# Performance work log

Measured on AMD Instinct MI355X. Metric: run time of the kernel, lower is better.

## Reference

```python
import jax, jax.numpy as jnp
import numpy as np
import math

N = 50000          # n_nodes
E = 1600000        # n_edges (avg degree 32)
D = 256            # input_size
H = 8              # n_heads
HS = D // H        # head_size = 32


def setup_inputs() -> dict:
    key = jax.random.key(0)
    k1, k2, k3, k4, k5 = jax.random.split(key, 5)
    X = jax.random.normal(k1, (N, D), dtype=jnp.float32)
    # xavier_uniform for [D, HS] weight: bound = sqrt(6 / (fan_in + fan_out))
    bound = math.sqrt(6.0 / (D + HS))
    Wq = jax.random.uniform(k2, (D, HS), jnp.float32, -bound, bound)
    Wk = jax.random.uniform(k3, (D, HS), jnp.float32, -bound, bound)
    Wv = jax.random.uniform(k4, (D, HS), jnp.float32, -bound, bound)
    edge_index = jax.random.randint(k5, (2, E), 0, N, dtype=jnp.int32)
    return {"X": X, "Wq": Wq, "Wk": Wk, "Wv": Wv, "edge_index": edge_index}


def reference(X, Wq, Wk, Wv, edge_index):
    # Projections: [N, HS]
    Q = X @ Wq
    K = X @ Wk
    V = X @ Wv
    r = edge_index[0]  # row (query) node per edge
    c = edge_index[1]  # col (key/value) node per edge
    dk = jnp.asarray(math.sqrt(HS), dtype=X.dtype)
    # Edge-level attention logits: [E]
    scores = jnp.sum(Q[r] * K[c], axis=-1) / dk
    # Sparse row-wise (dim=1) softmax over existing edges only.
    row_max = jax.ops.segment_max(scores, r, num_segments=N)   # -inf for empty rows
    ex = jnp.exp(scores - row_max[r])                          # [E]
    denom = jax.ops.segment_sum(ex, r, num_segments=N)         # [N]
    # Weighted V aggregation: [N, HS]
    num = jax.ops.segment_sum(ex[:, None] * V[c], r, num_segments=N)
    # Rows with no incident edges produce zeros (matches sparse softmax + to_dense @ V).
    safe = jnp.maximum(denom, jnp.asarray(1e-30, X.dtype))[:, None]
    return jnp.where(denom[:, None] > 0, num / safe, jnp.zeros_like(num))
```

## Files before the change

### kernel.cpp

```cpp
#include <hip/hip_runtime.h>

#define N_NODES 50000
#define N_EDGES 1600000
#define D_IN    256
#define HS      32

#define NB      400
#define ROWS_PB 125
#define CAP     5120
#define EPB     4096

#define MTILE   64
#define XPITCH  264

typedef __bf16 bf16x8 __attribute__((ext_vector_type(8)));
typedef float  floatx4 __attribute__((ext_vector_type(4)));

static __device__ __forceinline__ unsigned short f2bf(float f) {
    unsigned u = __float_as_uint(f);
    return (unsigned short)((u + 0x7FFFu + ((u >> 16) & 1u)) >> 16);
}

__global__ __launch_bounds__(256) void wfrag_kernel(
    const float* __restrict__ Wq, const float* __restrict__ Wk,
    const float* __restrict__ Wv, unsigned short* __restrict__ wfrag)
{
    const int i = blockIdx.x * blockDim.x + threadIdx.x;
    if (i >= 8 * 6 * 64 * 8) return;
    const int j    = i & 7;
    const int lane = (i >> 3) & 63;
    const int st   = i >> 9;
    const int t    = st % 6;
    const int s    = st / 6;
    const int k    = s * 32 + (lane >> 4) * 8 + j;
    const int col  = t * 16 + (lane & 15);
    float v;
    if      (col < 32) v = Wq[k * HS + col];
    else if (col < 64) v = Wk[k * HS + (col - 32)];
    else               v = Wv[k * HS + (col - 64)];
    wfrag[i] = f2bf(v);
}

__global__ __launch_bounds__(256) void proj_mfma_kernel(
    const float* __restrict__ X, const unsigned short* __restrict__ wfrag,
    float* __restrict__ Q, unsigned int* __restrict__ KVp)
{
    __shared__ unsigned short xs[MTILE * XPITCH];

    const int t    = threadIdx.x;
    const int lane = t & 63;
    const int w    = t >> 6;
    const int quad = lane >> 4;
    const int m16  = lane & 15;
    const int row0 = blockIdx.x * MTILE;

#pragma unroll
    for (int it = 0; it < (MTILE * 64) / 256; it++) {
        const int idx = it * 256 + t;
        const int r   = idx >> 6;
        const int c4  = idx & 63;
        int gr = row0 + r;
        if (gr >= N_NODES) gr = N_NODES - 1;
        const float4 xv = *(const float4*)(X + (size_t)gr * D_IN + c4 * 4);
        ushort4 b;
        b.x = f2bf(xv.x); b.y = f2bf(xv.y); b.z = f2bf(xv.z); b.w = f2bf(xv.w);
        *(ushort4*)(&xs[r * XPITCH + c4 * 4]) = b;
    }
    __syncthreads();

    floatx4 acc[6];
#pragma unroll
    for (int nt = 0; nt < 6; nt++) acc[nt] = (floatx4)0.f;

    const int arow = w * 16 + m16;

#pragma unroll
    for (int s = 0; s < 8; s++) {
        bf16x8 bfr[6];
#pragma unroll
        for (int nt = 0; nt < 6; nt++)
            bfr[nt] = *(const bf16x8*)(wfrag + (((s * 6 + nt) * 64 + lane) * 8));
        const bf16x8 afr = *(const bf16x8*)(&xs[arow * XPITCH + s * 32 + quad * 8]);
#pragma unroll
        for (int nt = 0; nt < 6; nt++)
            acc[nt] = __builtin_amdgcn_mfma_f32_16x16x32_bf16(afr, bfr[nt], acc[nt], 0, 0, 0);
    }

#pragma unroll
    for (int i = 0; i < 4; i++) {
        const int gr = row0 + w * 16 + quad * 4 + i;
        if (gr < N_NODES) {
#pragma unroll
            for (int nt = 0; nt < 2; nt++)
                Q[gr * HS + nt * 16 + m16] = acc[nt][i];
#pragma unroll
            for (int p = 0; p < 2; p++) {
                const int j = p * 16 + m16;
                const unsigned kb = f2bf(acc[2 + p][i]);
                const unsigned vb = f2bf(acc[4 + p][i]);
                KVp[gr * HS + j] = (kb << 16) | vb;
            }
        }
    }
}

__global__ __launch_bounds__(256) void bin_kernel(
    const int* __restrict__ er, const int* __restrict__ ec,
    int* __restrict__ fill, unsigned int* __restrict__ pairs)
{
    __shared__ int lcnt[NB];
    const int t  = threadIdx.x;
    const int e0 = blockIdx.x * EPB;
    const int e1 = min(e0 + EPB, N_EDGES);

    for (int b = t; b < NB; b += 256) lcnt[b] = 0;
    __syncthreads();

    for (int e = e0 + t; e < e1; e += 256)
        atomicAdd(&lcnt[er[e] / ROWS_PB], 1);
    __syncthreads();

    for (int b = t; b < NB; b += 256) {
        const int c = lcnt[b];
        lcnt[b] = (c > 0) ? atomicAdd(&fill[b], c) : 0;
    }
    __syncthreads();

    for (int e = e0 + t; e < e1; e += 256) {
        const int r = er[e];
        const int b = r / ROWS_PB;
        const int slot = atomicAdd(&lcnt[b], 1);
        pairs[(size_t)b * CAP + slot] =
            ((unsigned)(r - b * ROWS_PB) << 16) | (unsigned)ec[e];
    }
}

__global__ __launch_bounds__(512) void scanfill_kernel(
    const int* __restrict__ fill, int* __restrict__ bstart,
    int* __restrict__ rowptr)
{
    __shared__ int s[512];
    const int t = threadIdx.x;
    const int v = (t < NB) ? fill[t] : 0;
    s[t] = v;
    __syncthreads();
#pragma unroll
    for (int ofs = 1; ofs < 512; ofs <<= 1) {
        const int u = (t >= ofs) ? s[t - ofs] : 0;
        __syncthreads();
        s[t] += u;
        __syncthreads();
    }
    if (t < NB) bstart[t] = s[t] - v;
    if (t == 0) rowptr[N_NODES] = N_EDGES;
}

__global__ __launch_bounds__(256) void place_kernel(
    const unsigned int* __restrict__ pairs, const int* __restrict__ fill,
    const int* __restrict__ bstart, int* __restrict__ rowptr,
    int* __restrict__ col_sorted)
{
    __shared__ int cnt_l[ROWS_PB];
    __shared__ int s[128];
    __shared__ int stage[CAP];

    const int b = blockIdx.x;
    const int t = threadIdx.x;
    const int n = fill[b];
    const int base = bstart[b];
    const unsigned int* pb = pairs + (size_t)b * CAP;

    for (int i = t; i < ROWS_PB; i += 256) cnt_l[i] = 0;
    __syncthreads();

    for (int i = t; i < n; i += 256)
        atomicAdd(&cnt_l[pb[i] >> 16], 1);
    __syncthreads();

    if (t < 128) s[t] = (t < ROWS_PB) ? cnt_l[t] : 0;
    __syncthreads();
#pragma unroll
    for (int ofs = 1; ofs < 128; ofs <<= 1) {
        const int u = (t < 128 && t >= ofs) ? s[t - ofs] : 0;
        __syncthreads();
        if (t < 128) s[t] += u;
        __syncthreads();
    }
    int excl = 0;
    if (t < ROWS_PB) {
        excl = s[t] - cnt_l[t];
        rowptr[b * ROWS_PB + t] = base + excl;
    }
    __syncthreads();
    if (t < ROWS_PB) cnt_l[t] = excl;
    __syncthreads();

    for (int i = t; i < n; i += 256) {
        const unsigned p = pb[i];
        const int pos = atomicAdd(&cnt_l[p >> 16], 1);
        stage[pos] = (int)(p & 0xFFFFu);
    }
    __syncthreads();

    for (int i = t; i < n; i += 256)
        col_sorted[base + i] = stage[i];
}

__global__ __launch_bounds__(256) void aggregate_kernel(
    const int* __restrict__ rowptr, const int* __restrict__ col,
    const float* __restrict__ Q, const unsigned int* __restrict__ KVp,
    float* __restrict__ out)
{
    const int lane = threadIdx.x & 63;
    const int r    = (blockIdx.x * blockDim.x + threadIdx.x) >> 6;
    if (r >= N_NODES) return;
    const int comp = lane & 7;
    const int slot = lane >> 3;

    const float4 q4 = *(const float4*)(Q + r * HS + comp * 4);
    const int start = rowptr[r];
    const int end   = rowptr[r + 1];
    const float scale = 0.17677669529663687f;

    float accD = 0.f;
    float n0 = 0.f, n1 = 0.f, n2 = 0.f, n3 = 0.f;

    for (int e0 = start; e0 < end; e0 += 16) {
        const int last = end - 1;
        const int eA = e0 + slot;
        const int eB = e0 + 8 + slot;
        const int cA = col[min(eA, last)];
        const int cB = col[min(eB, last)];
        const uint4 kvA = *(const uint4*)(KVp + (size_t)cA * HS + comp * 4);
        const uint4 kvB = *(const uint4*)(KVp + (size_t)cB * HS + comp * 4);

        float pA = q4.x * __uint_as_float(kvA.x & 0xFFFF0000u)
                 + q4.y * __uint_as_float(kvA.y & 0xFFFF0000u)
                 + q4.z * __uint_as_float(kvA.z & 0xFFFF0000u)
                 + q4.w * __uint_as_float(kvA.w & 0xFFFF0000u);
        float pB = q4.x * __uint_as_float(kvB.x & 0xFFFF0000u)
                 + q4.y * __uint_as_float(kvB.y & 0xFFFF0000u)
                 + q4.z * __uint_as_float(kvB.z & 0xFFFF0000u)
                 + q4.w * __uint_as_float(kvB.w & 0xFFFF0000u);
#pragma unroll
        for (int ofs = 1; ofs < 8; ofs <<= 1) {
            pA += __shfl_xor(pA, ofs, 64);
            pB += __shfl_xor(pB, ofs, 64);
        }
        const float exA = (eA < end) ? __expf(pA * scale) : 0.f;
        const float exB = (eB < end) ? __expf(pB * scale) : 0.f;
        accD += exA + exB;
        n0 += exA * __uint_as_float(kvA.x << 16) + exB * __uint_as_float(kvB.x << 16);
        n1 += exA * __uint_as_float(kvA.y << 16) + exB * __uint_as_float(kvB.y << 16);
        n2 += exA * __uint_as_float(kvA.z << 16) + exB * __uint_as_float(kvB.z << 16);
        n3 += exA * __uint_as_float(kvA.w << 16) + exB * __uint_as_float(kvB.w << 16);
    }

#pragma unroll
    for (int ofs = 8; ofs < 64; ofs <<= 1) {
        accD += __shfl_xor(accD, ofs, 64);
        n0 += __shfl_xor(n0, ofs, 64);
        n1 += __shfl_xor(n1, ofs, 64);
        n2 += __shfl_xor(n2, ofs, 64);
        n3 += __shfl_xor(n3, ofs, 64);
    }

    if (slot == 0) {
        const float inv = (accD > 0.f) ? 1.f / accD : 0.f;
        float4 o;
        o.x = n0 * inv; o.y = n1 * inv; o.z = n2 * inv; o.w = n3 * inv;
        *(float4*)(out + r * HS + comp * 4) = o;
    }
}

extern "C" void kernel_launch(void* const* d_in, const int* in_sizes, int n_in,
                              void* d_out, int out_size, void* d_ws, size_t ws_size,
                              hipStream_t stream)
{
    const float* X  = (const float*)d_in[0];
    const float* Wq = (const float*)d_in[1];
    const float* Wk = (const float*)d_in[2];
    const float* Wv = (const float*)d_in[3];
    const int*   ei = (const int*)d_in[4];
    const int* er = ei;
    const int* ec = ei + N_EDGES;

    float* out = (float*)d_out;

    float* Q          = (float*)d_ws;
    unsigned int* KVp = (unsigned int*)(Q + (size_t)N_NODES * HS);
    int* fill         = (int*)(KVp + (size_t)N_NODES * HS);
    int* bstart       = fill + NB;
    int* rowptr       = bstart + NB;
    unsigned short* wfrag = (unsigned short*)(rowptr + (N_NODES + 1));
    unsigned int* pairs   = (unsigned int*)(wfrag + 8 * 6 * 64 * 8);
    int* col_sorted   = (int*)(pairs + (size_t)NB * CAP);

    hipMemsetAsync(fill, 0, NB * sizeof(int), stream);

    wfrag_kernel<<<(8 * 6 * 64 * 8 + 255) / 256, 256, 0, stream>>>(Wq, Wk, Wv, wfrag);
    proj_mfma_kernel<<<(N_NODES + MTILE - 1) / MTILE, 256, 0, stream>>>(X, wfrag, Q, KVp);

    bin_kernel<<<(N_EDGES + EPB - 1) / EPB, 256, 0, stream>>>(er, ec, fill, pairs);
    scanfill_kernel<<<1, 512, 0, stream>>>(fill, bstart, rowptr);
    place_kernel<<<NB, 256, 0, stream>>>(pairs, fill, bstart, rowptr, col_sorted);

    aggregate_kernel<<<(N_NODES * 64 + 255) / 256, 256, 0, stream>>>(
        rowptr, col_sorted, Q, KVp, out);
}
```

Measured before the change: 177.3 us.

## Fold memset into wfrag kernel, cache edges in registers, deepen aggregate loads

Drops the separate memset and does the fill-counter zeroing and the rowptr sentinel write inside wfrag_kernel. bin_kernel and place_kernel keep each thread's edges in register arrays so the second pass does not reload them from global memory. aggregate_kernel now processes 32 edges per iteration and issues four independent gathers before computing, which gives more memory-level parallelism. The fixed register arrays (16 and 20 entries) assume EPB and CAP bounds and raise register pressure.

```diff
diff --git a/kernel.cpp b/kernel.cpp
--- a/kernel.cpp
+++ b/kernel.cpp
@@ -23,8 +23,13 @@
 
 __global__ __launch_bounds__(256) void wfrag_kernel(
     const float* __restrict__ Wq, const float* __restrict__ Wk,
-    const float* __restrict__ Wv, unsigned short* __restrict__ wfrag)
-{
+    const float* __restrict__ Wv, unsigned short* __restrict__ wfrag,
+    int* __restrict__ fill, int* __restrict__ rowptr)
+{
+    if (blockIdx.x == 0) {
+        for (int b = threadIdx.x; b < NB; b += 256) fill[b] = 0;
+        if (threadIdx.x == 0) rowptr[N_NODES] = N_EDGES;
+    }
     const int i = blockIdx.x * blockDim.x + threadIdx.x;
     if (i >= 8 * 6 * 64 * 8) return;
     const int j    = i & 7;
@@ -116,8 +121,16 @@
     for (int b = t; b < NB; b += 256) lcnt[b] = 0;
     __syncthreads();
 
-    for (int e = e0 + t; e < e1; e += 256)
-        atomicAdd(&lcnt[er[e] / ROWS_PB], 1);
+    int rl[16], cl[16];
+#pragma unroll
+    for (int i = 0; i < 16; i++) {
+        const int e = e0 + t + i * 256;
+        if (e < e1) {
+            rl[i] = er[e];
+            cl[i] = ec[e];
+            atomicAdd(&lcnt[rl[i] / ROWS_PB], 1);
+        }
+    }
     __syncthreads();
 
     for (int b = t; b < NB; b += 256) {
@@ -126,18 +139,21 @@
     }
     __syncthreads();
 
-    for (int e = e0 + t; e < e1; e += 256) {
-        const int r = er[e];
-        const int b = r / ROWS_PB;
-        const int slot = atomicAdd(&lcnt[b], 1);
-        pairs[(size_t)b * CAP + slot] =
-            ((unsigned)(r - b * ROWS_PB) << 16) | (unsigned)ec[e];
+#pragma unroll
+    for (int i = 0; i < 16; i++) {
+        const int e = e0 + t + i * 256;
+        if (e < e1) {
+            const int r = rl[i];
+            const int b = r / ROWS_PB;
+            const int slot = atomicAdd(&lcnt[b], 1);
+            pairs[(size_t)b * CAP + slot] =
+                ((unsigned)(r - b * ROWS_PB) << 16) | (unsigned)cl[i];
+        }
     }
 }
 
 __global__ __launch_bounds__(512) void scanfill_kernel(
-    const int* __restrict__ fill, int* __restrict__ bstart,
-    int* __restrict__ rowptr)
+    const int* __restrict__ fill, int* __restrict__ bstart)
 {
     __shared__ int s[512];
     const int t = threadIdx.x;
@@ -152,7 +168,6 @@
         __syncthreads();
     }
     if (t < NB) bstart[t] = s[t] - v;
-    if (t == 0) rowptr[N_NODES] = N_EDGES;
 }
 
 __global__ __launch_bounds__(256) void place_kernel(
@@ -173,8 +188,15 @@
     for (int i = t; i < ROWS_PB; i += 256) cnt_l[i] = 0;
     __syncthreads();
 
-    for (int i = t; i < n; i += 256)
-        atomicAdd(&cnt_l[pb[i] >> 16], 1);
+    unsigned pl[20];
+#pragma unroll
+    for (int k = 0; k < 20; k++) {
+        const int i = t + k * 256;
+        if (i < n) {
+            pl[k] = pb[i];
+            atomicAdd(&cnt_l[pl[k] >> 16], 1);
+        }
+    }
     __syncthreads();
 
     if (t < 128) s[t] = (t < ROWS_PB) ? cnt_l[t] : 0;
@@ -195,10 +217,14 @@
     if (t < ROWS_PB) cnt_l[t] = excl;
     __syncthreads();
 
-    for (int i = t; i < n; i += 256) {
-        const unsigned p = pb[i];
-        const int pos = atomicAdd(&cnt_l[p >> 16], 1);
-        stage[pos] = (int)(p & 0xFFFFu);
+#pragma unroll
+    for (int k = 0; k < 20; k++) {
+        const int i = t + k * 256;
+        if (i < n) {
+            const unsigned p = pl[k];
+            const int pos = atomicAdd(&cnt_l[p >> 16], 1);
+            stage[pos] = (int)(p & 0xFFFFu);
+        }
     }
     __syncthreads();
 
@@ -220,40 +246,41 @@
     const float4 q4 = *(const float4*)(Q + r * HS + comp * 4);
     const int start = rowptr[r];
     const int end   = rowptr[r + 1];
+    const int last  = end - 1;
     const float scale = 0.17677669529663687f;
 
     float accD = 0.f;
     float n0 = 0.f, n1 = 0.f, n2 = 0.f, n3 = 0.f;
 
-    for (int e0 = start; e0 < end; e0 += 16) {
-        const int last = end - 1;
-        const int eA = e0 + slot;
-        const int eB = e0 + 8 + slot;
-        const int cA = col[min(eA, last)];
-        const int cB = col[min(eB, last)];
-        const uint4 kvA = *(const uint4*)(KVp + (size_t)cA * HS + comp * 4);
-        const uint4 kvB = *(const uint4*)(KVp + (size_t)cB * HS + comp * 4);
-
-        float pA = q4.x * __uint_as_float(kvA.x & 0xFFFF0000u)
-                 + q4.y * __uint_as_float(kvA.y & 0xFFFF0000u)
-                 + q4.z * __uint_as_float(kvA.z & 0xFFFF0000u)
-                 + q4.w * __uint_as_float(kvA.w & 0xFFFF0000u);
-        float pB = q4.x * __uint_as_float(kvB.x & 0xFFFF0000u)
-                 + q4.y * __uint_as_float(kvB.y & 0xFFFF0000u)
-                 + q4.z * __uint_as_float(kvB.z & 0xFFFF0000u)
-                 + q4.w * __uint_as_float(kvB.w & 0xFFFF0000u);
-#pragma unroll
-        for (int ofs = 1; ofs < 8; ofs <<= 1) {
-            pA += __shfl_xor(pA, ofs, 64);
-            pB += __shfl_xor(pB, ofs, 64);
-        }
-        const float exA = (eA < end) ? __expf(pA * scale) : 0.f;
-        const float exB = (eB < end) ? __expf(pB * scale) : 0.f;
-        accD += exA + exB;
-        n0 += exA * __uint_as_float(kvA.x << 16) + exB * __uint_as_float(kvB.x << 16);
-        n1 += exA * __uint_as_float(kvA.y << 16) + exB * __uint_as_float(kvB.y << 16);
-        n2 += exA * __uint_as_float(kvA.z << 16) + exB * __uint_as_float(kvB.z << 16);
-        n3 += exA * __uint_as_float(kvA.w << 16) + exB * __uint_as_float(kvB.w << 16);
+    for (int e0 = start; e0 < end; e0 += 32) {
+        int   cc[4];
+        uint4 kv[4];
+#pragma unroll
+        for (int b = 0; b < 4; b++)
+            if (e0 + 8 * b < end)
+                cc[b] = col[min(e0 + 8 * b + slot, last)];
+#pragma unroll
+        for (int b = 0; b < 4; b++)
+            if (e0 + 8 * b < end)
+                kv[b] = *(const uint4*)(KVp + (size_t)cc[b] * HS + comp * 4);
+#pragma unroll
+        for (int b = 0; b < 4; b++) {
+            if (e0 + 8 * b < end) {
+                float p = q4.x * __uint_as_float(kv[b].x & 0xFFFF0000u)
+                        + q4.y * __uint_as_float(kv[b].y & 0xFFFF0000u)
+                        + q4.z * __uint_as_float(kv[b].z & 0xFFFF0000u)
+                        + q4.w * __uint_as_float(kv[b].w & 0xFFFF0000u);
+#pragma unroll
+                for (int ofs = 1; ofs < 8; ofs <<= 1)
+                    p += __shfl_xor(p, ofs, 64);
+                const float ex = (e0 + 8 * b + slot < end) ? __expf(p * scale) : 0.f;
+                accD += ex;
+                n0 += ex * __uint_as_float(kv[b].x << 16);
+                n1 += ex * __uint_as_float(kv[b].y << 16);
+                n2 += ex * __uint_as_float(kv[b].z << 16);
+                n3 += ex * __uint_as_float(kv[b].w << 16);
+            }
+        }
     }
 
 #pragma unroll
@@ -296,13 +323,12 @@
     unsigned int* pairs   = (unsigned int*)(wfrag + 8 * 6 * 64 * 8);
     int* col_sorted   = (int*)(pairs + (size_t)NB * CAP);
 
-    hipMemsetAsync(fill, 0, NB * sizeof(int), stream);
-
-    wfrag_kernel<<<(8 * 6 * 64 * 8 + 255) / 256, 256, 0, stream>>>(Wq, Wk, Wv, wfrag);
+    wfrag_kernel<<<(8 * 6 * 64 * 8 + 255) / 256, 256, 0, stream>>>(
+        Wq, Wk, Wv, wfrag, fill, rowptr);
     proj_mfma_kernel<<<(N_NODES + MTILE - 1) / MTILE, 256, 0, stream>>>(X, wfrag, Q, KVp);
 
     bin_kernel<<<(N_EDGES + EPB - 1) / EPB, 256, 0, stream>>>(er, ec, fill, pairs);
-    scanfill_kernel<<<1, 512, 0, stream>>>(fill, bstart, rowptr);
+    scanfill_kernel<<<1, 512, 0, stream>>>(fill, bstart);
     place_kernel<<<NB, 256, 0, stream>>>(pairs, fill, bstart, rowptr, col_sorted);
 
     aggregate_kernel<<<(N_NODES * 64 + 255) / 256, 256, 0, stream>>>(
```

New measurement: 165.5 us. 6.7% less time.
